# Performance work log

Hardware: AMD Instinct MI355X
Metric: run time of the kernel (lower is better)

Reference implementation:

```python
import jax, jax.numpy as jnp
import numpy as np

N = 100000      # nodes per node type (asset, zone)
E = 1000000     # edges per edge type
HID = 64        # hidden_dim
HEADS = 2
CH = HID // HEADS  # 32, GATConv out_channels per head
L = 2           # num_layers
A = 64          # action_count
NG = 6          # global features
FW = 2 * HID + NG  # 134 feature width for heads


def _gat(xs_in, xd_in, W, a_src, a_dst, bias, src, dst, n_dst):
    """PyG GATConv (v1, add_self_loops=False, concat=True) for one edge type.
    xs_in: [Ns, HID] source feats, xd_in: [Nd, HID] dest feats (same lin weight W).
    Returns [n_dst, HEADS*CH]."""
    xs = (xs_in @ W).reshape(-1, HEADS, CH)
    xd = (xd_in @ W).reshape(-1, HEADS, CH)
    al_s = jnp.einsum('nhc,hc->nh', xs, a_src)
    al_d = jnp.einsum('nhc,hc->nh', xd, a_dst)
    al = jax.nn.leaky_relu(al_s[src] + al_d[dst], 0.2)       # [E, H]
    mx = jax.ops.segment_max(al, dst, num_segments=n_dst)    # segment softmax (stable)
    mx = jnp.where(jnp.isfinite(mx), mx, 0.0)                # empty segments
    ex = jnp.exp(al - mx[dst])
    den = jax.ops.segment_sum(ex, dst, num_segments=n_dst)
    w = ex / (den[dst] + 1e-16)                              # PyG softmax eps
    msg = xs[src] * w[:, :, None]                            # [E, H, C]
    out = jax.ops.segment_sum(msg.reshape(msg.shape[0], HEADS * CH), dst, num_segments=n_dst)
    return out + bias


def setup_inputs() -> dict:
    key = jax.random.key(0)
    ks = jax.random.split(key, 24)
    s = 0.05
    inp = {
        'x_asset': jax.random.normal(ks[0], (N, 16), jnp.float32),
        'x_zone': jax.random.normal(ks[1], (N, 32), jnp.float32),
        'ei_zz': jax.random.randint(ks[2], (2, E), 0, N, dtype=jnp.int32),
        'ei_az': jax.random.randint(ks[3], (2, E), 0, N, dtype=jnp.int32),
        'ei_za': jax.random.randint(ks[4], (2, E), 0, N, dtype=jnp.int32),
        'gvec': jax.random.uniform(ks[5], (NG,), jnp.float32),
        'mask': jax.random.randint(ks[6], (A,), 0, 2) == 1,
        'proj_W_asset': jax.random.normal(ks[7], (16, HID), jnp.float32) * s,
        'proj_b_asset': jnp.zeros((HID,), jnp.float32),
        'proj_W_zone': jax.random.normal(ks[8], (32, HID), jnp.float32) * s,
        'proj_b_zone': jnp.zeros((HID,), jnp.float32),
        'gat_W': jax.random.normal(ks[9], (L, 3, HID, HID), jnp.float32) * s,
        'gat_asrc': jax.random.normal(ks[10], (L, 3, HEADS, CH), jnp.float32) * s,
        'gat_adst': jax.random.normal(ks[11], (L, 3, HEADS, CH), jnp.float32) * s,
        'gat_bias': jnp.zeros((L, 3, HID), jnp.float32),
        'actor_W1': jax.random.normal(ks[12], (FW, HID), jnp.float32) * s,
        'actor_b1': jnp.zeros((HID,), jnp.float32),
        'actor_W2': jax.random.normal(ks[13], (HID, A), jnp.float32) * s,
        'actor_b2': jnp.zeros((A,), jnp.float32),
        'critic_W1': jax.random.normal(ks[14], (FW, HID), jnp.float32) * s,
        'critic_b1': jnp.zeros((HID,), jnp.float32),
        'critic_W2': jax.random.normal(ks[15], (HID, 1), jnp.float32) * s,
        'critic_b2': jnp.zeros((1,), jnp.float32),
    }
    return inp


def reference(x_asset, x_zone, ei_zz, ei_az, ei_za, gvec, mask,
              proj_W_asset, proj_b_asset, proj_W_zone, proj_b_zone,
              gat_W, gat_asrc, gat_adst, gat_bias,
              actor_W1, actor_b1, actor_W2, actor_b2,
              critic_W1, critic_b1, critic_W2, critic_b2):
    # input projections per node type
    ha = x_asset @ proj_W_asset + proj_b_asset   # [N, HID]
    hz = x_zone @ proj_W_zone + proj_b_zone      # [N, HID]
    # HeteroConv stack: edge types 0=(zone,near,zone) 1=(asset,in,zone) 2=(zone,contains,asset), aggr='sum'
    for l in range(L):
        z_zz = _gat(hz, hz, gat_W[l, 0], gat_asrc[l, 0], gat_adst[l, 0], gat_bias[l, 0], ei_zz[0], ei_zz[1], N)
        z_az = _gat(ha, hz, gat_W[l, 1], gat_asrc[l, 1], gat_adst[l, 1], gat_bias[l, 1], ei_az[0], ei_az[1], N)
        a_za = _gat(hz, ha, gat_W[l, 2], gat_asrc[l, 2], gat_adst[l, 2], gat_bias[l, 2], ei_za[0], ei_za[1], N)
        hz = jax.nn.relu(z_zz + z_az)
        ha = jax.nn.relu(a_za)
    # mean pool per node type, sorted order: asset, zone
    pooled = jnp.concatenate([ha.mean(axis=0), hz.mean(axis=0)])
    feats = jnp.concatenate([pooled, gvec])      # [FW]
    logits = jax.nn.relu(feats @ actor_W1 + actor_b1) @ actor_W2 + actor_b2   # [A]
    value = jax.nn.relu(feats @ critic_W1 + critic_b1) @ critic_W2 + critic_b2  # [1]
    m = jnp.where(mask.any(), mask, jnp.ones_like(mask))
    masked = jnp.where(m, logits, -jnp.inf)
    return jnp.concatenate([masked, value])      # [A+1]: masked logits + value
```

## Files before the change

### kernel.cpp

```cpp
#include <hip/hip_runtime.h>
#include <math.h>

#define CE 8192
#define BSH 9
#define BMAXB 512
#define ASTR 104
#define DSTR 72

typedef __attribute__((ext_vector_type(8))) short bf16x8;
typedef __attribute__((ext_vector_type(4))) float f32x4;
typedef __attribute__((ext_vector_type(2))) float f32x2;

__device__ __forceinline__ unsigned short f2bf(float f) {
    unsigned u = __float_as_uint(f);
    u += 0x7fffu + ((u >> 16) & 1u);
    return (unsigned short)(u >> 16);
}
__device__ __forceinline__ float bf2f(unsigned short u) {
    return __uint_as_float(((unsigned)u) << 16);
}

__global__ __launch_bounds__(256) void gemm_k(const float* __restrict__ X,
                                              const float* __restrict__ W,
                                              const float* __restrict__ bias,
                                              unsigned short* __restrict__ outb,
                                              int n, int kshift) {
    const int K = 1 << kshift;
    __shared__ float sXt[64 * 68];
    __shared__ float sW[64 * 64];
    __shared__ float sB[64];
    const int tid = threadIdx.x;
    const int row0 = blockIdx.x * 64;

    for (int i = tid * 4; i < 64 * K; i += 1024) {
        int r = i >> kshift, k = i & (K - 1);
        int row = row0 + r;
        float4 v = make_float4(0.f, 0.f, 0.f, 0.f);
        if (row < n) v = *(const float4*)(X + (size_t)row * K + k);
        sXt[(k + 0) * 68 + r] = v.x;
        sXt[(k + 1) * 68 + r] = v.y;
        sXt[(k + 2) * 68 + r] = v.z;
        sXt[(k + 3) * 68 + r] = v.w;
    }
    for (int i = tid * 4; i < K * 64; i += 1024)
        *(float4*)(sW + i) = *(const float4*)(W + i);
    if (tid < 64) sB[tid] = bias[tid];
    __syncthreads();

    const int tc = tid & 15, tr = tid >> 4;
    float acc[4][4] = {};
#pragma unroll 8
    for (int k = 0; k < K; ++k) {
        float4 a = *(const float4*)(sXt + k * 68 + tr * 4);
        float4 b = *(const float4*)(sW + k * 64 + tc * 4);
        acc[0][0] += a.x * b.x; acc[0][1] += a.x * b.y; acc[0][2] += a.x * b.z; acc[0][3] += a.x * b.w;
        acc[1][0] += a.y * b.x; acc[1][1] += a.y * b.y; acc[1][2] += a.y * b.z; acc[1][3] += a.y * b.w;
        acc[2][0] += a.z * b.x; acc[2][1] += a.z * b.y; acc[2][2] += a.z * b.z; acc[2][3] += a.z * b.w;
        acc[3][0] += a.w * b.x; acc[3][1] += a.w * b.y; acc[3][2] += a.w * b.z; acc[3][3] += a.w * b.w;
    }
#pragma unroll
    for (int i = 0; i < 4; ++i) {
        int row = row0 + tr * 4 + i;
        if (row < n) {
            float4 o;
            o.x = acc[i][0] + sB[tc * 4 + 0];
            o.y = acc[i][1] + sB[tc * 4 + 1];
            o.z = acc[i][2] + sB[tc * 4 + 2];
            o.w = acc[i][3] + sB[tc * 4 + 3];
            ushort4 v4 = make_ushort4(f2bf(o.x), f2bf(o.y), f2bf(o.z), f2bf(o.w));
            *(ushort4*)(outb + (size_t)row * 64 + tc * 4) = v4;
        }
    }
}

__global__ void wprep_k(const float* __restrict__ gW, unsigned short* __restrict__ Wbt) {
    int b = blockIdx.x;
    int t = threadIdx.x;
    for (int i = t; i < 4096; i += 256) {
        int nn = i >> 6, k = i & 63;
        Wbt[(size_t)b * 4096 + i] = f2bf(gW[(size_t)b * 4096 + k * 64 + nn]);
    }
}

__global__ __launch_bounds__(256) void gemm_mfma3_k(const unsigned short* __restrict__ hzb,
                                                    const unsigned short* __restrict__ hab,
                                                    const unsigned short* __restrict__ WbtL,
                                                    const float* __restrict__ gasL,
                                                    const float* __restrict__ Wd3,
                                                    unsigned char* __restrict__ ts0,
                                                    unsigned char* __restrict__ ts1,
                                                    unsigned char* __restrict__ ts2,
                                                    float2* __restrict__ als0,
                                                    float2* __restrict__ als1,
                                                    float2* __restrict__ als2,
                                                    float2* __restrict__ ald_zz,
                                                    float2* __restrict__ ald_az,
                                                    float2* __restrict__ ald_za, int n) {
    const int et = blockIdx.y;
    const unsigned short* Xb = (et == 1) ? hab : hzb;
    const unsigned short* Wt = WbtL + (size_t)et * 4096;
    const float* asrc = gasL + et * 64;
    unsigned char* ts8 = (et == 0) ? ts0 : (et == 1) ? ts1 : ts2;
    float2* alsOut = (et == 0) ? als0 : (et == 1) ? als1 : als2;

    __shared__ unsigned short sA[64 * ASTR];
    __shared__ unsigned short sB[64 * ASTR];
    __shared__ float sAs[64];
    __shared__ float sWd[384];
    const int tid = threadIdx.x;
    const int row0 = blockIdx.x * 64;

    for (int i = tid; i < 512; i += 256) {
        int r = i >> 3, seg = i & 7;
        int row = row0 + r;
        uint4 v = make_uint4(0, 0, 0, 0);
        if (row < n) v = *(const uint4*)(Xb + (size_t)row * 64 + seg * 8);
        *(uint4*)(sA + r * ASTR + seg * 8) = v;
    }
    for (int i = tid; i < 512; i += 256) {
        int nn = i >> 3, seg = i & 7;
        *(uint4*)(sB + nn * ASTR + seg * 8) = *(const uint4*)(Wt + nn * 64 + seg * 8);
    }
    if (tid < 64) sAs[tid] = asrc[tid];
    for (int i = tid; i < 384; i += 256) sWd[i] = Wd3[i];
    __syncthreads();

    const int lane = tid & 63;
    const int w = tid >> 6;
    const int m = lane & 15, q = lane >> 4;

    bf16x8 a0 = *(const bf16x8*)(sA + (w * 16 + m) * ASTR + q * 8);
    bf16x8 a1 = *(const bf16x8*)(sA + (w * 16 + m) * ASTR + 32 + q * 8);
    f32x4 acc[4];
#pragma unroll
    for (int c = 0; c < 4; ++c) {
        bf16x8 b0 = *(const bf16x8*)(sB + (c * 16 + m) * ASTR + q * 8);
        bf16x8 b1 = *(const bf16x8*)(sB + (c * 16 + m) * ASTR + 32 + q * 8);
        f32x4 z = {0.f, 0.f, 0.f, 0.f};
        z = __builtin_amdgcn_mfma_f32_16x16x32_bf16(a0, b0, z, 0, 0, 0);
        z = __builtin_amdgcn_mfma_f32_16x16x32_bf16(a1, b1, z, 0, 0, 0);
        acc[c] = z;
    }
    float s0[4], s1[4];
#pragma unroll
    for (int r = 0; r < 4; ++r) {
        s0[r] = acc[0][r] * sAs[m] + acc[1][r] * sAs[16 + m];
        s1[r] = acc[2][r] * sAs[32 + m] + acc[3][r] * sAs[48 + m];
    }
#pragma unroll
    for (int off = 1; off < 16; off <<= 1) {
#pragma unroll
        for (int r = 0; r < 4; ++r) { s0[r] += __shfl_xor(s0[r], off); s1[r] += __shfl_xor(s1[r], off); }
    }
    if (m < 4) {
        int row = row0 + w * 16 + q * 4 + m;
        if (row < n) alsOut[row] = make_float2(s0[m], s1[m]);
    }

    if (et != 2) {
        const int rid = tid >> 2, part = tid & 3;
        const int row = row0 + rid;
        const unsigned short* rp = sA + rid * ASTR + part * 16;
        bf16x8 x0 = *(const bf16x8*)rp;
        bf16x8 x1 = *(const bf16x8*)(rp + 8);
        float xv[16];
#pragma unroll
        for (int i = 0; i < 8; ++i) {
            xv[i]     = bf2f((unsigned short)x0[i]);
            xv[8 + i] = bf2f((unsigned short)x1[i]);
        }
        const float* wd = sWd + (et == 0 ? 0 : 256);
        float p0 = 0.f, p1 = 0.f, t0 = 0.f, t1 = 0.f;
#pragma unroll
        for (int i = 0; i < 16; ++i) {
            int k = part * 16 + i;
            p0 += xv[i] * wd[2 * k];
            p1 += xv[i] * wd[2 * k + 1];
        }
        if (et == 0) {
#pragma unroll
            for (int i = 0; i < 16; ++i) {
                int k = part * 16 + i;
                t0 += xv[i] * sWd[128 + 2 * k];
                t1 += xv[i] * sWd[128 + 2 * k + 1];
            }
        }
        p0 += __shfl_xor(p0, 1); p0 += __shfl_xor(p0, 2);
        p1 += __shfl_xor(p1, 1); p1 += __shfl_xor(p1, 2);
        t0 += __shfl_xor(t0, 1); t0 += __shfl_xor(t0, 2);
        t1 += __shfl_xor(t1, 1); t1 += __shfl_xor(t1, 2);
        if (part == 0 && row < n) {
            if (et == 0) {
                ald_zz[row] = make_float2(p0, p1);
                ald_az[row] = make_float2(t0, t1);
            } else {
                ald_za[row] = make_float2(p0, p1);
            }
        }
    }

    __syncthreads();
    unsigned char* sD = (unsigned char*)sA;
#pragma unroll
    for (int c = 0; c < 4; ++c) {
        int pk01 = __builtin_amdgcn_cvt_pk_fp8_f32(acc[c][0], acc[c][1], 0, false);
        int pk23 = __builtin_amdgcn_cvt_pk_fp8_f32(acc[c][2], acc[c][3], 0, false);
        int rb = w * 16 + q * 4;
        int col = c * 16 + m;
        sD[(rb + 0) * DSTR + col] = (unsigned char)(pk01 & 0xff);
        sD[(rb + 1) * DSTR + col] = (unsigned char)((pk01 >> 8) & 0xff);
        sD[(rb + 2) * DSTR + col] = (unsigned char)(pk23 & 0xff);
        sD[(rb + 3) * DSTR + col] = (unsigned char)((pk23 >> 8) & 0xff);
    }
    __syncthreads();
    for (int i = tid; i < 512; i += 256) {
        int r = i >> 3, seg = i & 7;
        int row = row0 + r;
        if (row < n)
            *(uint2*)(ts8 + (size_t)row * 64 + seg * 8) = *(const uint2*)(sD + r * DSTR + seg * 8);
    }
}

__global__ void wd3_k(const float* __restrict__ gW, const float* __restrict__ gad,
                      float* __restrict__ Wd3All) {
    int l = blockIdx.x;
    int t = threadIdx.x;
    int et = t >> 7, r = t & 127;
    int k = r >> 1, h = r & 1;
    const float* W = gW + (size_t)l * 3 * 4096 + et * 4096;
    const float* adst = gad + (size_t)l * 3 * 64 + et * 64;
    float s = 0.f;
    for (int c = 0; c < 32; ++c) s += W[k * 64 + h * 32 + c] * adst[h * 32 + c];
    Wd3All[l * 384 + t] = s;
}

__global__ __launch_bounds__(1024) void chunk_hist_k(const int* __restrict__ e0p,
                                                     const int* __restrict__ e1p,
                                                     const int* __restrict__ e2p,
                                                     int* __restrict__ cnt,
                                                     int E, int CB, int NBr) {
    int b = blockIdx.x;
    int et = b / CB, c = b - et * CB;
    const int* dst = (et == 0 ? e0p : et == 1 ? e1p : e2p) + E;
    __shared__ int lcnt[BMAXB];
    int t = threadIdx.x;
    for (int i = t; i < NBr; i += 1024) lcnt[i] = 0;
    __syncthreads();
    int base = c * CE;
    for (int i = t; i < CE; i += 1024) {
        int e = base + i;
        if (e < E) atomicAdd(&lcnt[dst[e] >> BSH], 1);
    }
    __syncthreads();
    int rowbase = et * NBr;
    for (int i = t; i < NBr; i += 1024) cnt[(size_t)(rowbase + i) * CB + c] = lcnt[i];
}
__global__ __launch_bounds__(256) void row_scan_k(int* __restrict__ cnt,
                                                  int* __restrict__ btot, int CB) {
    size_t row = (size_t)blockIdx.x * CB;
    __shared__ int buf[512];
    int t = threadIdx.x;
    int o0 = (t < CB) ? cnt[row + t] : 0;
    int o1 = (t + 256 < CB) ? cnt[row + t + 256] : 0;
    buf[t] = o0; buf[t + 256] = o1;
    __syncthreads();
    for (int off = 1; off < 512; off <<= 1) {
        int v0 = (t >= off) ? buf[t - off] : 0;
        int v1 = (t + 256 >= off) ? buf[t + 256 - off] : 0;
        __syncthreads();
        buf[t] += v0; buf[t + 256] += v1;
        __syncthreads();
    }
    if (t < CB) cnt[row + t] = buf[t] - o0;
    if (t + 256 < CB) cnt[row + t + 256] = buf[t + 256] - o1;
    if (t == 0) btot[blockIdx.x] = buf[511];
}
__global__ __launch_bounds__(1024) void btot_scan_k(const int* __restrict__ btot,
                                                    int* __restrict__ bbase,
                                                    int* __restrict__ bOff,
                                                    int NT, int E,
                                                    int* __restrict__ rowptrAll, int N) {
    __shared__ int buf[1024];
    int t = threadIdx.x;
    int v = (t < NT) ? btot[t] : 0;
    buf[t] = v;
    __syncthreads();
    for (int off = 1; off < 1024; off <<= 1) {
        int u = (t >= off) ? buf[t - off] : 0;
        __syncthreads();
        buf[t] += u;
        __syncthreads();
    }
    if (t < NT) { int e = buf[t] - v; bbase[t] = e; bOff[t] = e; }
    if (t == 0) {
        bOff[NT] = 3 * E;
        rowptrAll[N] = E;
        rowptrAll[(N + 1) + N] = 2 * E;
        rowptrAll[2 * (N + 1) + N] = 3 * E;
    }
}
__global__ __launch_bounds__(1024) void chunk_scatter_k(const int* __restrict__ e0p,
                                                        const int* __restrict__ e1p,
                                                        const int* __restrict__ e2p,
                                                        const int* __restrict__ cnt,
                                                        const int* __restrict__ bbase,
                                                        int* __restrict__ pairs,
                                                        int E, int CB, int NBr) {
    int b = blockIdx.x;
    int et = b / CB, c = b - et * CB;
    const int* eb = (et == 0 ? e0p : et == 1 ? e1p : e2p);
    __shared__ int lcur[BMAXB];
    int t = threadIdx.x;
    int rb = et * NBr;
    for (int i = t; i < NBr; i += 1024) lcur[i] = bbase[rb + i] + cnt[(size_t)(rb + i) * CB + c];
    __syncthreads();
    int base = c * CE;
    for (int i = t; i < CE; i += 1024) {
        int e = base + i;
        if (e < E) {
            int d = eb[E + e];
            int pos = atomicAdd(&lcur[d >> BSH], 1);
            pairs[pos] = ((d & (BMAXB - 1)) << 20) | eb[e];
        }
    }
}
__global__ __launch_bounds__(256) void bucket_local_k(const int* __restrict__ pairs,
                                                      const int* __restrict__ bOff,
                                                      int* __restrict__ rowptrAll,
                                                      int* __restrict__ ssrc, int N, int NBr) {
    int b = blockIdx.x;
    int et = b / NBr, lb = b - et * NBr;
    int beg = bOff[b], end = bOff[b + 1];
    int node0 = lb << BSH;
    int* rowptr = rowptrAll + (size_t)et * (N + 1);
    __shared__ int deg[512], cur[512];
    int t = threadIdx.x;
    deg[t] = 0; deg[t + 256] = 0;
    __syncthreads();
    for (int j = beg + t; j < end; j += 256)
        atomicAdd(&deg[pairs[j] >> 20], 1);
    __syncthreads();
    int o0 = deg[t], o1 = deg[t + 256];
    __syncthreads();
    for (int off = 1; off < 512; off <<= 1) {
        int v0 = (t >= off) ? deg[t - off] : 0;
        int v1 = (t + 256 >= off) ? deg[t + 256 - off] : 0;
        __syncthreads();
        deg[t] += v0; deg[t + 256] += v1;
        __syncthreads();
    }
    int e0 = beg + deg[t] - o0, e1 = beg + deg[t + 256] - o1;
    cur[t] = e0; cur[t + 256] = e1;
    int n0 = node0 + t, n1 = node0 + t + 256;
    if (n0 < N) rowptr[n0] = e0;
    if (n1 < N) rowptr[n1] = e1;
    __syncthreads();
    for (int j = beg + t; j < end; j += 256) {
        int p = pairs[j];
        int pos = atomicAdd(&cur[p >> 20], 1);
        ssrc[pos] = p & 0xFFFFF;
    }
}

__global__ __launch_bounds__(256) void gat_out2_k(const int* __restrict__ rowptr0,
                                                  const int* __restrict__ rowptr1,
                                                  const int* __restrict__ rowptr2,
                                                  const int* __restrict__ ssrc,
                                                  const float2* __restrict__ als0,
                                                  const float2* __restrict__ ald0,
                                                  const unsigned char* __restrict__ ts0,
                                                  const float2* __restrict__ als1,
                                                  const float2* __restrict__ ald1,
                                                  const unsigned char* __restrict__ ts1,
                                                  const float2* __restrict__ als2,
                                                  const float2* __restrict__ ald2,
                                                  const unsigned char* __restrict__ ts2,
                                                  const float* __restrict__ gbL,
                                                  unsigned short* __restrict__ outHz,
                                                  unsigned short* __restrict__ outHa,
                                                  int n) {
    const int y = blockIdx.y;
    const int nseg = y ? 1 : 2;
    int lane = threadIdx.x & 63;
    int gl = lane & 15;
    int wid = blockIdx.x * 16 + (threadIdx.x >> 4);
    if (wid >= n) return;
    const int r = gl >> 3;
    const int c0 = (gl & 7) * 8;
    const int gbase = lane & 48;

    float acc8[8] = {};
    for (int seg = 0; seg < nseg; ++seg) {
        const int* rowptr;
        const float2 *als, *ald;
        const unsigned char* ts8;
        if (y) { rowptr = rowptr2; als = als2; ald = ald2; ts8 = ts2; }
        else if (seg == 0) { rowptr = rowptr0; als = als0; ald = ald0; ts8 = ts0; }
        else { rowptr = rowptr1; als = als1; ald = ald1; ts8 = ts1; }
        int beg = rowptr[wid], end = rowptr[wid + 1];
        if (beg == end) continue;
        float2 bd = ald[wid];
        float d0 = 0.f, d1 = 0.f;
        float a8[8] = {};
        for (int cbeg = beg; cbeg < end; cbeg += 16) {
            int j = cbeg + gl;
            int s = 0; float e0 = 0.f, e1 = 0.f;
            if (j < end) {
                s = ssrc[j];
                float2 a = als[s];
                float l0 = a.x + bd.x; l0 = l0 > 0.f ? l0 : 0.2f * l0;
                float l1 = a.y + bd.y; l1 = l1 > 0.f ? l1 : 0.2f * l1;
                e0 = __expf(l0); e1 = __expf(l1);
            }
            d0 += e0; d1 += e1;
            int cnt = min(16, end - cbeg);
            uint2 rr[8]; float wv[8];
#pragma unroll
            for (int k = 0; k < 8; ++k) {
                int jj = 2 * k;
                if (jj < cnt) {
                    int srcLane = gbase + jj + r;
                    int sj = __shfl(s, srcLane);
                    float w0 = __shfl(e0, srcLane), w1 = __shfl(e1, srcLane);
                    float w = (c0 < 32) ? w0 : w1;
                    bool live = (jj + r) < cnt;
                    wv[k] = live ? w : 0.f;
                    if (live) rr[k] = *(const uint2*)(ts8 + (size_t)sj * 64 + c0);
                    else rr[k] = make_uint2(0, 0);
                } else { wv[k] = 0.f; rr[k] = make_uint2(0, 0); }
            }
#pragma unroll
            for (int k = 0; k < 8; ++k) {
                float w = wv[k];
                if (w != 0.f) {
                    f32x2 p0 = __builtin_amdgcn_cvt_pk_f32_fp8(rr[k].x, false);
                    f32x2 p1 = __builtin_amdgcn_cvt_pk_f32_fp8(rr[k].x, true);
                    f32x2 p2 = __builtin_amdgcn_cvt_pk_f32_fp8(rr[k].y, false);
                    f32x2 p3 = __builtin_amdgcn_cvt_pk_f32_fp8(rr[k].y, true);
                    a8[0] += p0.x * w; a8[1] += p0.y * w;
                    a8[2] += p1.x * w; a8[3] += p1.y * w;
                    a8[4] += p2.x * w; a8[5] += p2.y * w;
                    a8[6] += p3.x * w; a8[7] += p3.y * w;
                }
            }
        }
#pragma unroll
        for (int off = 1; off < 16; off <<= 1) { d0 += __shfl_xor(d0, off); d1 += __shfl_xor(d1, off); }
#pragma unroll
        for (int i = 0; i < 8; ++i) a8[i] += __shfl_xor(a8[i], 8);
        float inv = (c0 < 32) ? 1.f / (d0 + 1e-16f) : 1.f / (d1 + 1e-16f);
#pragma unroll
        for (int i = 0; i < 8; ++i) acc8[i] += a8[i] * inv;
    }

    if (r == 0) {
        const float* biasA = y ? gbL + 128 : gbL;
        const float* biasB = y ? nullptr : gbL + 64;
        float4 bA1 = *(const float4*)(biasA + c0);
        float4 bA2 = *(const float4*)(biasA + c0 + 4);
        float b8[8] = { bA1.x, bA1.y, bA1.z, bA1.w, bA2.x, bA2.y, bA2.z, bA2.w };
        if (biasB) {
            float4 bB1 = *(const float4*)(biasB + c0);
            float4 bB2 = *(const float4*)(biasB + c0 + 4);
            b8[0] += bB1.x; b8[1] += bB1.y; b8[2] += bB1.z; b8[3] += bB1.w;
            b8[4] += bB2.x; b8[5] += bB2.y; b8[6] += bB2.z; b8[7] += bB2.w;
        }
        float v8[8];
#pragma unroll
        for (int i = 0; i < 8; ++i) v8[i] = fmaxf(acc8[i] + b8[i], 0.f);
        unsigned short* outBf = y ? outHa : outHz;
        unsigned short* bp = outBf + (size_t)wid * 64 + c0;
        ushort4 u1 = make_ushort4(f2bf(v8[0]), f2bf(v8[1]), f2bf(v8[2]), f2bf(v8[3]));
        ushort4 u2 = make_ushort4(f2bf(v8[4]), f2bf(v8[5]), f2bf(v8[6]), f2bf(v8[7]));
        *(ushort4*)bp = u1;
        *(ushort4*)(bp + 4) = u2;
    }
}

__global__ __launch_bounds__(256) void pool_k(const unsigned short* __restrict__ hab,
                                              const unsigned short* __restrict__ hzb,
                                              float* __restrict__ sums, int n) {
    __shared__ float red[2][16][64];
    int tid = threadIdx.x;
    int c4 = (tid & 15) * 4;
    int rq = tid >> 4;
    float la[4] = {}, lz[4] = {};
    for (int row = blockIdx.x * 16 + rq; row < n; row += gridDim.x * 16) {
        ushort4 va = *(const ushort4*)(hab + (size_t)row * 64 + c4);
        ushort4 vz = *(const ushort4*)(hzb + (size_t)row * 64 + c4);
        la[0] += bf2f(va.x); la[1] += bf2f(va.y); la[2] += bf2f(va.z); la[3] += bf2f(va.w);
        lz[0] += bf2f(vz.x); lz[1] += bf2f(vz.y); lz[2] += bf2f(vz.z); lz[3] += bf2f(vz.w);
    }
#pragma unroll
    for (int i = 0; i < 4; ++i) { red[0][rq][c4 + i] = la[i]; red[1][rq][c4 + i] = lz[i]; }
    __syncthreads();
    if (tid < 64) {
        float ta = 0.f, tz = 0.f;
#pragma unroll
        for (int rr = 0; rr < 16; ++rr) { ta += red[0][rr][tid]; tz += red[1][rr][tid]; }
        atomicAdd(sums + tid, ta);
        atomicAdd(sums + 64 + tid, tz);
    }
}

__global__ __launch_bounds__(64) void head_k(const float* __restrict__ sums,
                                             const float* __restrict__ gvec,
                                             const unsigned char* __restrict__ mask,
                                             const float* __restrict__ aW1, const float* __restrict__ ab1,
                                             const float* __restrict__ aW2, const float* __restrict__ ab2,
                                             const float* __restrict__ cW1, const float* __restrict__ cb1,
                                             const float* __restrict__ cW2, const float* __restrict__ cb2,
                                             float* __restrict__ out, float invn) {
    __shared__ float f[134];
    __shared__ float h1a[64];
    int t = threadIdx.x;
    f[t] = sums[t] * invn;
    f[64 + t] = sums[64 + t] * invn;
    if (t < 6) f[128 + t] = gvec[t];
    __syncthreads();
    float a = ab1[t], c = cb1[t];
    for (int i = 0; i < 134; ++i) {
        float fv = f[i];
        a += fv * aW1[i * 64 + t];
        c += fv * cW1[i * 64 + t];
    }
    h1a[t] = fmaxf(a, 0.f);
    float vp = fmaxf(c, 0.f) * cW2[t];
    __syncthreads();
    float lg = ab2[t];
    for (int j = 0; j < 64; ++j) lg += h1a[j] * aW2[j * 64 + t];
    for (int off = 32; off; off >>= 1) vp += __shfl_down(vp, off);
    unsigned char mb = mask[t];
    unsigned long long bal = __ballot(mb != 0);
    float ov = (bal == 0ull || mb) ? lg : -3.0e38f;
    out[t] = ov;
    if (t == 0) out[64] = vp + cb2[0];
}

extern "C" void kernel_launch(void* const* d_in, const int* in_sizes, int n_in,
                              void* d_out, int out_size, void* d_ws, size_t ws_size,
                              hipStream_t stream) {
    const float* x_asset = (const float*)d_in[0];
    const float* x_zone  = (const float*)d_in[1];
    const int* ei[3] = { (const int*)d_in[2], (const int*)d_in[3], (const int*)d_in[4] };
    const float* gvec = (const float*)d_in[5];
    const unsigned char* mask = (const unsigned char*)d_in[6];
    const float* pWa = (const float*)d_in[7];
    const float* pba = (const float*)d_in[8];
    const float* pWz = (const float*)d_in[9];
    const float* pbz = (const float*)d_in[10];
    const float* gW  = (const float*)d_in[11];
    const float* gas = (const float*)d_in[12];
    const float* gad = (const float*)d_in[13];
    const float* gb  = (const float*)d_in[14];
    const float* aW1 = (const float*)d_in[15];
    const float* ab1 = (const float*)d_in[16];
    const float* aW2 = (const float*)d_in[17];
    const float* ab2 = (const float*)d_in[18];
    const float* cW1 = (const float*)d_in[19];
    const float* cb1 = (const float*)d_in[20];
    const float* cW2 = (const float*)d_in[21];
    const float* cb2 = (const float*)d_in[22];

    const int N = in_sizes[0] / 16;
    const int E = in_sizes[2] / 2;
    const int NBr = (N + 511) >> BSH;
    const int CB  = (E + CE - 1) / CE;
    const int NT  = 3 * NBr;

    float* ws = (float*)d_ws;
    size_t off = 0;
    unsigned short* hab = (unsigned short*)(ws + off); off += (size_t)N * 32;
    unsigned short* hzb = (unsigned short*)(ws + off); off += (size_t)N * 32;
    unsigned char* ts3[3];
    for (int et = 0; et < 3; ++et) { ts3[et] = (unsigned char*)(ws + off); off += (size_t)N * 16; }
    float2* als3[3];
    for (int et = 0; et < 3; ++et) { als3[et] = (float2*)(ws + off); off += (size_t)2 * N; }
    float2* ald3[3];
    for (int et = 0; et < 3; ++et) { ald3[et] = (float2*)(ws + off); off += (size_t)2 * N; }
    unsigned short* Wbt = (unsigned short*)(ws + off); off += 12288 + 64;
    float* Wd3All = ws + off; off += 768;
    float* sums = ws + off; off += 128;
    int* rowptrAll = (int*)(ws + off); off += (size_t)3 * (N + 1);
    int* ssrcAll   = (int*)(ws + off); off += (size_t)3 * E;
    int* pairs     = (int*)(ws + off); off += (size_t)3 * E;
    int* cnt   = (int*)(ws + off); off += (size_t)NT * CB;
    int* btot  = (int*)(ws + off); off += 1024;
    int* bbase = (int*)(ws + off); off += 1024;
    int* bOff  = (int*)(ws + off); off += (size_t)(NT + 1);

    const int gGemm = (N + 63) / 64;
    const int gGat  = (N + 15) / 16;

    chunk_hist_k<<<3 * CB, 1024, 0, stream>>>(ei[0], ei[1], ei[2], cnt, E, CB, NBr);
    row_scan_k<<<NT, 256, 0, stream>>>(cnt, btot, CB);
    btot_scan_k<<<1, 1024, 0, stream>>>(btot, bbase, bOff, NT, E, rowptrAll, N);
    chunk_scatter_k<<<3 * CB, 1024, 0, stream>>>(ei[0], ei[1], ei[2], cnt, bbase, pairs, E, CB, NBr);
    bucket_local_k<<<NT, 256, 0, stream>>>(pairs, bOff, rowptrAll, ssrcAll, N, NBr);

    wprep_k<<<6, 256, 0, stream>>>(gW, Wbt);
    wd3_k<<<2, 384, 0, stream>>>(gW, gad, Wd3All);
    gemm_k<<<gGemm, 256, 0, stream>>>(x_asset, pWa, pba, hab, N, 4);
    gemm_k<<<gGemm, 256, 0, stream>>>(x_zone,  pWz, pbz, hzb, N, 5);

    for (int l = 0; l < 2; ++l) {
        gemm_mfma3_k<<<dim3(gGemm, 3), 256, 0, stream>>>(hzb, hab,
                                                         Wbt + (size_t)l * 3 * 4096,
                                                         gas + (size_t)l * 3 * 64,
                                                         Wd3All + (size_t)l * 384,
                                                         ts3[0], ts3[1], ts3[2],
                                                         als3[0], als3[1], als3[2],
                                                         ald3[0], ald3[1], ald3[2], N);
        gat_out2_k<<<dim3(gGat, 2), 256, 0, stream>>>(rowptrAll, rowptrAll + (N + 1),
                                                      rowptrAll + 2 * (N + 1), ssrcAll,
                                                      als3[0], ald3[0], ts3[0],
                                                      als3[1], ald3[1], ts3[1],
                                                      als3[2], ald3[2], ts3[2],
                                                      gb + (size_t)l * 3 * 64,
                                                      hzb, hab, N);
    }

    hipMemsetAsync(sums, 0, 128 * sizeof(float), stream);
    pool_k<<<256, 256, 0, stream>>>(hab, hzb, sums, N);
    head_k<<<1, 64, 0, stream>>>(sums, gvec, mask,
                                 aW1, ab1, aW2, ab2, cW1, cb1, cW2, cb2,
                                 (float*)d_out, 1.0f / (float)N);
}
```

Before: 428.1 us.

## Merge prep and projection launches, use wave-shuffle scan, packed FP8 accumulation

Folds the two weight-prep kernels into one launch and the two input projection GEMMs into one 2D-grid launch, cutting launch count. The bucket-local CSR build now runs 512 threads with a wavefront shuffle scan in place of a barrier-heavy shared-memory Hillis-Steele scan. The GAT aggregation drops the per-edge zero-weight branch, accumulates with packed float2 multiply-adds, and reads gathered FP8 rows with nontemporal loads. The gains in each part are small, and the nontemporal hint could hurt reuse of rows that are gathered repeatedly.

```diff
diff --git a/kernel.cpp b/kernel.cpp
--- a/kernel.cpp
+++ b/kernel.cpp
@@ -20,12 +20,23 @@
     return __uint_as_float(((unsigned)u) << 16);
 }
 
-__global__ __launch_bounds__(256) void gemm_k(const float* __restrict__ X,
-                                              const float* __restrict__ W,
-                                              const float* __restrict__ bias,
-                                              unsigned short* __restrict__ outb,
-                                              int n, int kshift) {
+__global__ __launch_bounds__(256) void gemm2_k(const float* __restrict__ Xa,
+                                               const float* __restrict__ Xz,
+                                               const float* __restrict__ Wa,
+                                               const float* __restrict__ Wz,
+                                               const float* __restrict__ ba,
+                                               const float* __restrict__ bz,
+                                               unsigned short* __restrict__ outa,
+                                               unsigned short* __restrict__ outz,
+                                               int n) {
+    const int y = blockIdx.y;
+    const float* X = y ? Xz : Xa;
+    const float* W = y ? Wz : Wa;
+    const float* bias = y ? bz : ba;
+    unsigned short* outb = y ? outz : outa;
+    const int kshift = y ? 5 : 4;
     const int K = 1 << kshift;
+
     __shared__ float sXt[64 * 68];
     __shared__ float sW[64 * 64];
     __shared__ float sB[64];
@@ -73,12 +84,24 @@
     }
 }
 
-__global__ void wprep_k(const float* __restrict__ gW, unsigned short* __restrict__ Wbt) {
+__global__ void prep_k(const float* __restrict__ gW, const float* __restrict__ gad,
+                       unsigned short* __restrict__ Wbt, float* __restrict__ Wd3All) {
     int b = blockIdx.x;
     int t = threadIdx.x;
-    for (int i = t; i < 4096; i += 256) {
-        int nn = i >> 6, k = i & 63;
-        Wbt[(size_t)b * 4096 + i] = f2bf(gW[(size_t)b * 4096 + k * 64 + nn]);
+    if (b < 6) {
+        for (int i = t; i < 4096; i += 384) {
+            int nn = i >> 6, k = i & 63;
+            Wbt[(size_t)b * 4096 + i] = f2bf(gW[(size_t)b * 4096 + k * 64 + nn]);
+        }
+    } else {
+        int l = b - 6;
+        int et = t >> 7, r = t & 127;
+        int k = r >> 1, h = r & 1;
+        const float* W = gW + (size_t)l * 3 * 4096 + et * 4096;
+        const float* adst = gad + (size_t)l * 3 * 64 + et * 64;
+        float s = 0.f;
+        for (int c = 0; c < 32; ++c) s += W[k * 64 + h * 32 + c] * adst[h * 32 + c];
+        Wd3All[l * 384 + t] = s;
     }
 }
 
@@ -221,19 +244,6 @@
     }
 }
 
-__global__ void wd3_k(const float* __restrict__ gW, const float* __restrict__ gad,
-                      float* __restrict__ Wd3All) {
-    int l = blockIdx.x;
-    int t = threadIdx.x;
-    int et = t >> 7, r = t & 127;
-    int k = r >> 1, h = r & 1;
-    const float* W = gW + (size_t)l * 3 * 4096 + et * 4096;
-    const float* adst = gad + (size_t)l * 3 * 64 + et * 64;
-    float s = 0.f;
-    for (int c = 0; c < 32; ++c) s += W[k * 64 + h * 32 + c] * adst[h * 32 + c];
-    Wd3All[l * 384 + t] = s;
-}
-
 __global__ __launch_bounds__(1024) void chunk_hist_k(const int* __restrict__ e0p,
                                                      const int* __restrict__ e1p,
                                                      const int* __restrict__ e2p,
@@ -324,7 +334,7 @@
         }
     }
 }
-__global__ __launch_bounds__(256) void bucket_local_k(const int* __restrict__ pairs,
+__global__ __launch_bounds__(512) void bucket_local_k(const int* __restrict__ pairs,
                                                       const int* __restrict__ bOff,
                                                       int* __restrict__ rowptrAll,
                                                       int* __restrict__ ssrc, int N, int NBr) {
@@ -333,29 +343,33 @@
     int beg = bOff[b], end = bOff[b + 1];
     int node0 = lb << BSH;
     int* rowptr = rowptrAll + (size_t)et * (N + 1);
-    __shared__ int deg[512], cur[512];
-    int t = threadIdx.x;
-    deg[t] = 0; deg[t + 256] = 0;
-    __syncthreads();
-    for (int j = beg + t; j < end; j += 256)
+    __shared__ int deg[512];
+    __shared__ int cur[512];
+    __shared__ int wsum[8];
+    int t = threadIdx.x, lane = t & 63, wq = t >> 6;
+    deg[t] = 0;
+    __syncthreads();
+    for (int j = beg + t; j < end; j += 512)
         atomicAdd(&deg[pairs[j] >> 20], 1);
     __syncthreads();
-    int o0 = deg[t], o1 = deg[t + 256];
-    __syncthreads();
-    for (int off = 1; off < 512; off <<= 1) {
-        int v0 = (t >= off) ? deg[t - off] : 0;
-        int v1 = (t + 256 >= off) ? deg[t + 256 - off] : 0;
-        __syncthreads();
-        deg[t] += v0; deg[t + 256] += v1;
-        __syncthreads();
-    }
-    int e0 = beg + deg[t] - o0, e1 = beg + deg[t + 256] - o1;
-    cur[t] = e0; cur[t + 256] = e1;
-    int n0 = node0 + t, n1 = node0 + t + 256;
+    int v = deg[t];
+    int x = v;
+#pragma unroll
+    for (int off = 1; off < 64; off <<= 1) {
+        int u = __shfl_up(x, off);
+        if (lane >= off) x += u;
+    }
+    if (lane == 63) wsum[wq] = x;
+    __syncthreads();
+    int basep = 0;
+#pragma unroll
+    for (int q = 0; q < 8; ++q) basep += (q < wq) ? wsum[q] : 0;
+    int e0 = beg + basep + x - v;
+    cur[t] = e0;
+    int n0 = node0 + t;
     if (n0 < N) rowptr[n0] = e0;
-    if (n1 < N) rowptr[n1] = e1;
-    __syncthreads();
-    for (int j = beg + t; j < end; j += 256) {
+    __syncthreads();
+    for (int j = beg + t; j < end; j += 512) {
         int p = pairs[j];
         int pos = atomicAdd(&cur[p >> 20], 1);
         ssrc[pos] = p & 0xFFFFF;
@@ -388,8 +402,9 @@
     const int r = gl >> 3;
     const int c0 = (gl & 7) * 8;
     const int gbase = lane & 48;
-
-    float acc8[8] = {};
+    const bool head0 = (c0 < 32);
+
+    f32x2 acc2[4] = {};
     for (int seg = 0; seg < nseg; ++seg) {
         const int* rowptr;
         const float2 *als, *ald;
@@ -401,7 +416,7 @@
         if (beg == end) continue;
         float2 bd = ald[wid];
         float d0 = 0.f, d1 = 0.f;
-        float a8[8] = {};
+        f32x2 a2[4] = {};
         for (int cbeg = beg; cbeg < end; cbeg += 16) {
             int j = cbeg + gl;
             int s = 0; float e0 = 0.f, e1 = 0.f;
@@ -422,38 +437,47 @@
                     int srcLane = gbase + jj + r;
                     int sj = __shfl(s, srcLane);
                     float w0 = __shfl(e0, srcLane), w1 = __shfl(e1, srcLane);
-                    float w = (c0 < 32) ? w0 : w1;
                     bool live = (jj + r) < cnt;
-                    wv[k] = live ? w : 0.f;
-                    if (live) rr[k] = *(const uint2*)(ts8 + (size_t)sj * 64 + c0);
-                    else rr[k] = make_uint2(0, 0);
+                    wv[k] = live ? (head0 ? w0 : w1) : 0.f;
+                    if (live) {
+                        unsigned long long v = __builtin_nontemporal_load(
+                            (const unsigned long long*)(ts8 + (size_t)sj * 64 + c0));
+                        rr[k].x = (unsigned)v;
+                        rr[k].y = (unsigned)(v >> 32);
+                    } else rr[k] = make_uint2(0, 0);
                 } else { wv[k] = 0.f; rr[k] = make_uint2(0, 0); }
             }
 #pragma unroll
             for (int k = 0; k < 8; ++k) {
                 float w = wv[k];
-                if (w != 0.f) {
-                    f32x2 p0 = __builtin_amdgcn_cvt_pk_f32_fp8(rr[k].x, false);
-                    f32x2 p1 = __builtin_amdgcn_cvt_pk_f32_fp8(rr[k].x, true);
-                    f32x2 p2 = __builtin_amdgcn_cvt_pk_f32_fp8(rr[k].y, false);
-                    f32x2 p3 = __builtin_amdgcn_cvt_pk_f32_fp8(rr[k].y, true);
-                    a8[0] += p0.x * w; a8[1] += p0.y * w;
-                    a8[2] += p1.x * w; a8[3] += p1.y * w;
-                    a8[4] += p2.x * w; a8[5] += p2.y * w;
-                    a8[6] += p3.x * w; a8[7] += p3.y * w;
-                }
+                f32x2 w2 = { w, w };
+                f32x2 p0 = __builtin_amdgcn_cvt_pk_f32_fp8(rr[k].x, false);
+                f32x2 p1 = __builtin_amdgcn_cvt_pk_f32_fp8(rr[k].x, true);
+                f32x2 p2 = __builtin_amdgcn_cvt_pk_f32_fp8(rr[k].y, false);
+                f32x2 p3 = __builtin_amdgcn_cvt_pk_f32_fp8(rr[k].y, true);
+                a2[0] += p0 * w2;
+                a2[1] += p1 * w2;
+                a2[2] += p2 * w2;
+                a2[3] += p3 * w2;
             }
         }
 #pragma unroll
         for (int off = 1; off < 16; off <<= 1) { d0 += __shfl_xor(d0, off); d1 += __shfl_xor(d1, off); }
 #pragma unroll
-        for (int i = 0; i < 8; ++i) a8[i] += __shfl_xor(a8[i], 8);
-        float inv = (c0 < 32) ? 1.f / (d0 + 1e-16f) : 1.f / (d1 + 1e-16f);
-#pragma unroll
-        for (int i = 0; i < 8; ++i) acc8[i] += a8[i] * inv;
+        for (int i = 0; i < 4; ++i) {
+            a2[i].x += __shfl_xor(a2[i].x, 8);
+            a2[i].y += __shfl_xor(a2[i].y, 8);
+        }
+        float inv = head0 ? 1.f / (d0 + 1e-16f) : 1.f / (d1 + 1e-16f);
+        f32x2 inv2 = { inv, inv };
+#pragma unroll
+        for (int i = 0; i < 4; ++i) acc2[i] += a2[i] * inv2;
     }
 
     if (r == 0) {
+        float acc8[8];
+#pragma unroll
+        for (int i = 0; i < 4; ++i) { acc8[2 * i] = acc2[i].x; acc8[2 * i + 1] = acc2[i].y; }
         const float* biasA = y ? gbL + 128 : gbL;
         const float* biasB = y ? nullptr : gbL + 64;
         float4 bA1 = *(const float4*)(biasA + c0);
@@ -596,12 +620,11 @@
     row_scan_k<<<NT, 256, 0, stream>>>(cnt, btot, CB);
     btot_scan_k<<<1, 1024, 0, stream>>>(btot, bbase, bOff, NT, E, rowptrAll, N);
     chunk_scatter_k<<<3 * CB, 1024, 0, stream>>>(ei[0], ei[1], ei[2], cnt, bbase, pairs, E, CB, NBr);
-    bucket_local_k<<<NT, 256, 0, stream>>>(pairs, bOff, rowptrAll, ssrcAll, N, NBr);
-
-    wprep_k<<<6, 256, 0, stream>>>(gW, Wbt);
-    wd3_k<<<2, 384, 0, stream>>>(gW, gad, Wd3All);
-    gemm_k<<<gGemm, 256, 0, stream>>>(x_asset, pWa, pba, hab, N, 4);
-    gemm_k<<<gGemm, 256, 0, stream>>>(x_zone,  pWz, pbz, hzb, N, 5);
+    bucket_local_k<<<NT, 512, 0, stream>>>(pairs, bOff, rowptrAll, ssrcAll, N, NBr);
+
+    prep_k<<<8, 384, 0, stream>>>(gW, gad, Wbt, Wd3All);
+    gemm2_k<<<dim3(gGemm, 2), 256, 0, stream>>>(x_asset, x_zone, pWa, pWz, pba, pbz,
+                                                hab, hzb, N);
 
     for (int l = 0; l < 2; ++l) {
         gemm_mfma3_k<<<dim3(gGemm, 3), 256, 0, stream>>>(hzb, hab,
```

After: 449.5 us. +5.0%, slower.
